# Kernel tuning notes

Measured on AMD Instinct MI355X. Metric: run time of the kernel, lower is better.

Reference implementation:

```python
import jax, jax.numpy as jnp
import numpy as np

B, T, D, H, K = 8, 1024, 512, 8, 33
DK = D // H
PAD = (K - 1) // 2
EPS = 1e-5


def _ln(x, g, b):
    m = x.mean(-1, keepdims=True)
    v = ((x - m) ** 2).mean(-1, keepdims=True)
    return (x - m) / jnp.sqrt(v + EPS) * g + b


def _ffn(x, g, b, w1, b1, w2, b2):
    h = jax.nn.silu(_ln(x, g, b) @ w1 + b1)
    return h @ w2 + b2


def _rel_shift(x):
    # x: [B, H, T1, T2]
    b, h, t1, t2 = x.shape
    x = jnp.pad(x, ((0, 0), (0, 0), (0, 0), (1, 0)))
    x = x.reshape(b, h, t2 + 1, t1)[:, :, 1:, :].reshape(b, h, t1, t2)
    return x[..., :t1]


def setup_inputs() -> dict:
    key = jax.random.key(0)
    ks = iter(jax.random.split(key, 40))
    rn = lambda *s: jax.random.normal(next(ks), s, jnp.float32) * 0.02
    inp = {
        'x': jax.random.normal(next(ks), (B, T, D), jnp.float32),
        'pos_emb': jax.random.normal(next(ks), (1, T, D), jnp.float32),
        # ffn1
        'ln1_g': jnp.ones((D,), jnp.float32), 'ln1_b': jnp.zeros((D,), jnp.float32),
        'ffn1_w1': rn(D, 4 * D), 'ffn1_b1': jnp.zeros((4 * D,), jnp.float32),
        'ffn1_w2': rn(4 * D, D), 'ffn1_b2': jnp.zeros((D,), jnp.float32),
        # mhsa
        'lnq_g': jnp.ones((D,), jnp.float32), 'lnq_b': jnp.zeros((D,), jnp.float32),
        'lnk_g': jnp.ones((D,), jnp.float32), 'lnk_b': jnp.zeros((D,), jnp.float32),
        'lnv_g': jnp.ones((D,), jnp.float32), 'lnv_b': jnp.zeros((D,), jnp.float32),
        'wq': rn(D, D), 'wk': rn(D, D), 'wv': rn(D, D), 'wpos': rn(D, D),
        'pos_bias_u': jnp.zeros((H, DK), jnp.float32),
        'pos_bias_v': jnp.zeros((H, DK), jnp.float32),
        'wfc': rn(D, D),
        # conv module
        'cln_g': jnp.ones((D,), jnp.float32), 'cln_b': jnp.zeros((D,), jnp.float32),
        'pw1': rn(D, 4 * D),             # pointwise_conv1 weight as [in, out]
        'dw_w': rn(2 * D, 1, K),         # depthwise conv weight [C, 1, K]
        'bn_g': jnp.ones((2 * D,), jnp.float32), 'bn_b': jnp.zeros((2 * D,), jnp.float32),
        'pw2': rn(2 * D, D),
        # ffn2
        'ln2_g': jnp.ones((D,), jnp.float32), 'ln2_b': jnp.zeros((D,), jnp.float32),
        'ffn2_w1': rn(D, 4 * D), 'ffn2_b1': jnp.zeros((4 * D,), jnp.float32),
        'ffn2_w2': rn(4 * D, D), 'ffn2_b2': jnp.zeros((D,), jnp.float32),
        # final layer norm
        'lnf_g': jnp.ones((D,), jnp.float32), 'lnf_b': jnp.zeros((D,), jnp.float32),
    }
    return inp


def reference(x, pos_emb, ln1_g, ln1_b, ffn1_w1, ffn1_b1, ffn1_w2, ffn1_b2,
              lnq_g, lnq_b, lnk_g, lnk_b, lnv_g, lnv_b, wq, wk, wv, wpos,
              pos_bias_u, pos_bias_v, wfc,
              cln_g, cln_b, pw1, dw_w, bn_g, bn_b, pw2,
              ln2_g, ln2_b, ffn2_w1, ffn2_b1, ffn2_w2, ffn2_b2, lnf_g, lnf_b):
    b, t, d = x.shape
    scale = 1.0 / DK ** 0.5

    # ---- FFN1 (half-step) ----
    out = 0.5 * x + 0.5 * (x + _ffn(x, ln1_g, ln1_b, ffn1_w1, ffn1_b1, ffn1_w2, ffn1_b2))

    # ---- rel-pos MHSA ----
    res = out
    q = (_ln(out, lnq_g, lnq_b) @ wq).reshape(b, t, H, DK)            # [B,T,H,dk]
    k = (_ln(out, lnk_g, lnk_b) @ wk).reshape(b, t, H, DK).transpose(0, 2, 1, 3)
    v = (_ln(out, lnv_g, lnv_b) @ wv).reshape(b, t, H, DK).transpose(0, 2, 1, 3)
    p = (pos_emb @ wpos).reshape(pos_emb.shape[0], -1, H, DK).transpose(0, 2, 3, 1)  # [1,H,dk,Tp]

    q_u = (q + pos_bias_u).transpose(0, 2, 1, 3)                      # [B,H,T,dk]
    q_v = (q + pos_bias_v).transpose(0, 2, 1, 3)
    matrix_bd = _rel_shift(jnp.matmul(q_v, p) * scale)                # [B,H,T,T]
    scores = jnp.einsum('bhqd,bhkd->bhqk', q_u, k) * scale + matrix_bd
    attn = jax.nn.softmax(scores, axis=-1)
    o = jnp.einsum('bhqk,bhkd->bhqd', attn, v)
    out = o.transpose(0, 2, 1, 3).reshape(b, t, d) @ wfc + res

    # ---- convolution module ----
    res = out
    h = _ln(out, cln_g, cln_b) @ pw1                                  # [B,T,4D]
    a, g = jnp.split(h, 2, axis=-1)
    h = a * jax.nn.sigmoid(g)                                         # GLU -> [B,T,2D]
    h = jax.lax.conv_general_dilated(
        h.transpose(0, 2, 1), dw_w, window_strides=(1,),
        padding=[(PAD, PAD)], feature_group_count=2 * D,
        dimension_numbers=('NCH', 'OIH', 'NCH')).transpose(0, 2, 1)
    h = jax.nn.silu(_ln(h, bn_g, bn_b))
    out = h @ pw2 + res

    # ---- FFN2 (half-step) + final LN ----
    out = 0.5 * out + 0.5 * (out + _ffn(out, ln2_g, ln2_b, ffn2_w1, ffn2_b1, ffn2_w2, ffn2_b2))
    return _ln(out, lnf_g, lnf_b)
```

## Files before the change

kernel.cpp:

```cpp
#include <hip/hip_runtime.h>

typedef unsigned short bf16u;
typedef __attribute__((ext_vector_type(8))) short bf16x8;
typedef __attribute__((ext_vector_type(4))) float f32x4;

__device__ __forceinline__ float bf2f(bf16u u) {
    return __uint_as_float(((unsigned)u) << 16);
}
__device__ __forceinline__ bf16u f2bf(float f) {
    unsigned u = __float_as_uint(f);
    unsigned r = (u + 0x7fffu + ((u >> 16) & 1u)) >> 16;
    return (bf16u)r;
}
__device__ __forceinline__ float sigmoidf_(float x) {
    return 1.0f / (1.0f + __expf(-x));
}

__device__ __forceinline__ void gload_lds16(const bf16u* g, bf16u* l) {
    __builtin_amdgcn_global_load_lds(
        (const __attribute__((address_space(1))) unsigned int*)(const void*)g,
        (__attribute__((address_space(3))) unsigned int*)(void*)l, 16, 0, 0);
}

__global__ void init_flag_kernel(int* flag) {
    if (threadIdx.x == 0 && blockIdx.x == 0) *flag = 0;
}
__global__ __launch_bounds__(256) void detect_kernel(
    const void* x, int nelem, int* flag)
{
    const int scan = nelem < (1 << 20) ? nelem : (1 << 20);
    const bf16u* p = (const bf16u*)x;
    int bad = 0;
    for (int j = blockIdx.x * 256 + threadIdx.x; j < scan; j += 65536) {
        unsigned u = p[j];
        if ((u & 0x7F80u) == 0x7F80u) bad = 1;
    }
    if (bad) atomicOr(flag, 1);
}

__global__ __launch_bounds__(256) void cvt_bf_kernel(
    const void* __restrict__ in, bf16u* __restrict__ out, int n,
    const int* __restrict__ flagp)
{
    const int f32 = *flagp;
    const int i = blockIdx.x * 256 + threadIdx.x;
    if (i >= n) return;
    if (f32) out[i] = f2bf(((const float*)in)[i]);
    else     out[i] = ((const bf16u*)in)[i];
}

__global__ __launch_bounds__(256) void wtrans_kernel(
    const void* __restrict__ W, bf16u* __restrict__ Wt, int K, int N,
    const int* __restrict__ flagp)
{
    __shared__ float tile[32][33];
    const int f32 = *flagp;
    const int n0 = blockIdx.x * 32, k0 = blockIdx.y * 32;
    const int tx = threadIdx.x & 31, ty = threadIdx.x >> 5;
    #pragma unroll
    for (int r = 0; r < 4; ++r) {
        const int k = ty + r * 8;
        float v;
        if (f32) v = ((const float*)W)[(size_t)(k0 + k) * N + n0 + tx];
        else     v = bf2f(((const bf16u*)W)[(size_t)(k0 + k) * N + n0 + tx]);
        tile[k][tx] = v;
    }
    __syncthreads();
    #pragma unroll
    for (int r = 0; r < 4; ++r) {
        const int n = ty + r * 8;
        Wt[(size_t)(n0 + n) * K + k0 + tx] = f2bf(tile[tx][n]);
    }
}

__global__ __launch_bounds__(256) void vtrans_kernel(
    const bf16u* __restrict__ vb, bf16u* __restrict__ vt)
{
    __shared__ bf16u tile[32][33];
    const int j0 = blockIdx.x * 32;
    const int h = blockIdx.y >> 1, dt = (blockIdx.y & 1) * 32;
    const int b = blockIdx.z;
    const int tx = threadIdx.x & 31, ty = threadIdx.x >> 5;
    #pragma unroll
    for (int r = 0; r < 4; ++r) {
        const int j = ty + r * 8;
        tile[j][tx] = vb[(size_t)(b * 1024 + j0 + j) * 512 + h * 64 + dt + tx];
    }
    __syncthreads();
    #pragma unroll
    for (int r = 0; r < 4; ++r) {
        const int d = ty + r * 8;
        vt[(size_t)((b * 8 + h) * 64 + dt + d) * 1024 + j0 + tx] = tile[tx][d];
    }
}

__global__ __launch_bounds__(256) void add_qbias_kernel(
    const bf16u* __restrict__ qb, const void* __restrict__ bu,
    const void* __restrict__ bv, bf16u* __restrict__ qu,
    bf16u* __restrict__ qv, const int* __restrict__ flagp)
{
    const int f32 = *flagp;
    const int idx = blockIdx.x * 256 + threadIdx.x;
    const int c = idx & 511;
    const float q = bf2f(qb[idx]);
    float ub, vbias;
    if (f32) { ub = ((const float*)bu)[c]; vbias = ((const float*)bv)[c]; }
    else     { ub = bf2f(((const bf16u*)bu)[c]); vbias = bf2f(((const bf16u*)bv)[c]); }
    qu[idx] = f2bf(q + ub);
    qv[idx] = f2bf(q + vbias);
}

template <int D, int IN_MODE, int OUT_MODE, bool SILU, bool COPY>
__global__ __launch_bounds__(256) void ln_kernel(
    const void* __restrict__ in_, const void* __restrict__ gvec,
    const void* __restrict__ bvec, void* __restrict__ out_,
    float* __restrict__ copy_out, const int* __restrict__ flagp)
{
    constexpr int VPT = D / 256;
    const int f32 = *flagp;
    const int row = blockIdx.x;
    const int tid = threadIdx.x;
    const size_t base = (size_t)row * D;
    float x[VPT];
    if (IN_MODE == 2 || (IN_MODE == 1 && !f32)) {
        const bf16u* in = (const bf16u*)in_;
        #pragma unroll
        for (int i = 0; i < VPT; ++i) x[i] = bf2f(in[base + tid + i * 256]);
    } else {
        const float* in = (const float*)in_;
        #pragma unroll
        for (int i = 0; i < VPT; ++i) x[i] = in[base + tid + i * 256];
    }
    float s = 0.f, q = 0.f;
    #pragma unroll
    for (int i = 0; i < VPT; ++i) { s += x[i]; q += x[i] * x[i]; }
    __shared__ float red[10];
    #pragma unroll
    for (int off = 32; off; off >>= 1) {
        s += __shfl_down(s, off, 64);
        q += __shfl_down(q, off, 64);
    }
    const int lane = tid & 63, wv = tid >> 6;
    if (lane == 0) { red[wv] = s; red[4 + wv] = q; }
    __syncthreads();
    if (tid == 0) {
        float ts = red[0] + red[1] + red[2] + red[3];
        float tq = red[4] + red[5] + red[6] + red[7];
        float mean = ts / (float)D;
        float var = tq / (float)D - mean * mean;
        red[8] = mean;
        red[9] = rsqrtf(var + 1e-5f);
    }
    __syncthreads();
    const float mean = red[8], rstd = red[9];
    #pragma unroll
    for (int i = 0; i < VPT; ++i) {
        const int c = tid + i * 256;
        float gv, bv;
        if (f32) {
            gv = ((const float*)gvec)[c];
            bv = ((const float*)bvec)[c];
        } else {
            gv = bf2f(((const bf16u*)gvec)[c]);
            bv = bf2f(((const bf16u*)bvec)[c]);
        }
        float v = (x[i] - mean) * rstd * gv + bv;
        if (SILU) v *= sigmoidf_(v);
        if (OUT_MODE == 0) {
            ((bf16u*)out_)[base + c] = f2bf(v);
        } else {
            if (f32) ((float*)out_)[base + c] = v;
            else     ((bf16u*)out_)[base + c] = f2bf(v);
        }
        if (COPY) copy_out[base + c] = x[i];
    }
}

template <int TM>
__global__ __launch_bounds__(256) void gemm_mfma(
    const bf16u* __restrict__ A, const bf16u* __restrict__ Wt,
    const void* __restrict__ bias, const float* __restrict__ res,
    void* __restrict__ C, int M, int N, int K, float alpha, int act,
    int outbf, const int* __restrict__ flagp)
{
    constexpr int CHUNKS_A = TM * 4;
    constexpr int TOT = CHUNKS_A + 512;
    constexpr int CPW = TOT / 4;
    constexpr int ISSUES = CPW / 64;
    constexpr int BUFSZ = (TM + 128) * 32;
    constexpr int MI = 4;
    constexpr int NJ = (TM == 128) ? 4 : 2;
    __shared__ bf16u sh[3 * BUFSZ];
    const int f32 = *flagp;
    const int tid = threadIdx.x;
    const int mtiles = M / TM;
    const int lid = blockIdx.y * gridDim.x + blockIdx.x;
    const int bm = (lid % mtiles) * TM;
    const int bn = (lid / mtiles) * 128;
    const int lane = tid & 63, wvid = tid >> 6;
    const int wm = (TM == 128) ? (wvid >> 1) * 64 : 0;
    const int wn = (TM == 128) ? (wvid & 1) * 64 : wvid * 32;

    f32x4 acc[MI][NJ];
    {
        f32x4 z = {0.f, 0.f, 0.f, 0.f};
        #pragma unroll
        for (int i = 0; i < MI; ++i)
            #pragma unroll
            for (int j = 0; j < NJ; ++j) acc[i][j] = z;
    }
    const int kq = (lane >> 4) * 8, fr = lane & 15;

    #define STAGE_G(k0, bufp)                                                   \
    {                                                                           \
        bf16u* base_ = (bufp);                                                  \
        _Pragma("unroll")                                                       \
        for (int t = 0; t < ISSUES; ++t) {                                      \
            const int cc = wvid * CPW + t * 64 + lane;                          \
            const bf16u* src_;                                                  \
            if (cc < CHUNKS_A)                                                  \
                src_ = A + (size_t)(bm + (cc >> 2)) * K + (k0) + (cc & 3) * 8;  \
            else {                                                              \
                const int cb_ = cc - CHUNKS_A;                                  \
                src_ = Wt + (size_t)(bn + (cb_ >> 2)) * K + (k0) + (cb_ & 3) * 8;\
            }                                                                   \
            gload_lds16(src_, base_ + (wvid * CPW + t * 64) * 8);               \
        }                                                                       \
    }

    const int KT = K / 32;
    STAGE_G(0, sh);
    STAGE_G(32, sh + BUFSZ);
    int bufidx = 0;
    for (int kt = 0; kt < KT; ++kt) {
        if (kt + 1 < KT)
            asm volatile("s_waitcnt vmcnt(%0)\ns_barrier" :: "i"(ISSUES) : "memory");
        else
            asm volatile("s_waitcnt vmcnt(0)\ns_barrier" ::: "memory");
        if (kt + 2 < KT) {
            int nb = bufidx + 2; if (nb >= 3) nb -= 3;
            STAGE_G((kt + 2) * 32, sh + nb * BUFSZ);
        }
        const bf16u* buf = sh + bufidx * BUFSZ;
        bf16x8 af[MI], bfr[NJ];
        #pragma unroll
        for (int i = 0; i < MI; ++i)
            af[i] = *(const bf16x8*)&buf[(wm + i * 16 + fr) * 32 + kq];
        #pragma unroll
        for (int j = 0; j < NJ; ++j)
            bfr[j] = *(const bf16x8*)&buf[TM * 32 + (wn + j * 16 + fr) * 32 + kq];
        #pragma unroll
        for (int i = 0; i < MI; ++i)
            #pragma unroll
            for (int j = 0; j < NJ; ++j)
                acc[i][j] = __builtin_amdgcn_mfma_f32_16x16x32_bf16(
                    af[i], bfr[j], acc[i][j], 0, 0, 0);
        ++bufidx; if (bufidx == 3) bufidx = 0;
    }
    #undef STAGE_G

    const int quad = lane >> 4, col = lane & 15;
    #pragma unroll
    for (int j = 0; j < NJ; ++j) {
        const int n = bn + wn + j * 16 + col;
        float bv = 0.f;
        if (bias) bv = f32 ? ((const float*)bias)[n]
                           : bf2f(((const bf16u*)bias)[n]);
        #pragma unroll
        for (int i = 0; i < MI; ++i) {
            #pragma unroll
            for (int r = 0; r < 4; ++r) {
                const int m = bm + wm + i * 16 + quad * 4 + r;
                float v = acc[i][j][r] + bv;
                if (act == 1) v *= sigmoidf_(v);
                v *= alpha;
                const size_t off = (size_t)m * N + n;
                if (res) v += res[off];
                if (outbf) ((bf16u*)C)[off] = f2bf(v);
                else       ((float*)C)[off] = v;
            }
        }
    }
}

__global__ __launch_bounds__(256) void attn_score_mfma(
    const bf16u* __restrict__ qu, const bf16u* __restrict__ qv,
    const bf16u* __restrict__ kb, const bf16u* __restrict__ pb,
    bf16u* __restrict__ S, bf16u* __restrict__ BD)
{
    constexpr int BUFSZ = 8192;
    __shared__ bf16u sh[2 * BUFSZ];
    const int tid = threadIdx.x;
    const int z = blockIdx.z;
    const int h = z & 7, bb = (z >> 3) & 1, which = z >> 4;
    const bf16u* A = (which ? qv : qu) + (size_t)bb * 524288;
    const bf16u* B = which ? pb : (kb + (size_t)bb * 524288);
    bf16u* C = (which ? BD : S) + (size_t)(bb * 8 + h) * 1048576;
    const int hoff = h * 64;
    const int bm = blockIdx.y * 128, bn = blockIdx.x * 128;
    const int lane = tid & 63, wvid = tid >> 6;
    const int wm = (wvid >> 1) * 64, wn = (wvid & 1) * 64;
    const int kq = (lane >> 4) * 8, fr = lane & 15;

    f32x4 acc[4][4];
    {
        f32x4 zr = {0.f, 0.f, 0.f, 0.f};
        #pragma unroll
        for (int i = 0; i < 4; ++i)
            #pragma unroll
            for (int j = 0; j < 4; ++j) acc[i][j] = zr;
    }

    #define STAGE_S(k0, bsel)                                                   \
    {                                                                           \
        bf16u* base_ = sh + (bsel) * BUFSZ;                                     \
        _Pragma("unroll")                                                       \
        for (int t = 0; t < 4; ++t) {                                           \
            const int cc = wvid * 256 + t * 64 + lane;                          \
            const bf16u* src_;                                                  \
            if (cc < 512)                                                       \
                src_ = A + (size_t)(bm + (cc >> 2)) * 512 + hoff + (k0) + (cc & 3) * 8; \
            else {                                                              \
                const int cb_ = cc - 512;                                       \
                src_ = B + (size_t)(bn + (cb_ >> 2)) * 512 + hoff + (k0) + (cb_ & 3) * 8; \
            }                                                                   \
            gload_lds16(src_, base_ + (wvid * 256 + t * 64) * 8);               \
        }                                                                       \
    }

    STAGE_S(0, 0);
    #pragma unroll
    for (int kt = 0; kt < 2; ++kt) {
        __syncthreads();
        if (kt == 0) STAGE_S(32, 1);
        const bf16u* buf = sh + (kt & 1) * BUFSZ;
        bf16x8 af[4], bfr[4];
        #pragma unroll
        for (int i = 0; i < 4; ++i)
            af[i] = *(const bf16x8*)&buf[(wm + i * 16 + fr) * 32 + kq];
        #pragma unroll
        for (int j = 0; j < 4; ++j)
            bfr[j] = *(const bf16x8*)&buf[4096 + (wn + j * 16 + fr) * 32 + kq];
        #pragma unroll
        for (int i = 0; i < 4; ++i)
            #pragma unroll
            for (int j = 0; j < 4; ++j)
                acc[i][j] = __builtin_amdgcn_mfma_f32_16x16x32_bf16(
                    af[i], bfr[j], acc[i][j], 0, 0, 0);
    }
    #undef STAGE_S

    const int quad = lane >> 4, col = lane & 15;
    #pragma unroll
    for (int j = 0; j < 4; ++j) {
        const int n = bn + wn + j * 16 + col;
        #pragma unroll
        for (int i = 0; i < 4; ++i) {
            #pragma unroll
            for (int r = 0; r < 4; ++r) {
                const int m = bm + wm + i * 16 + quad * 4 + r;
                C[(size_t)m * 1024 + n] = f2bf(acc[i][j][r] * 0.125f);
            }
        }
    }
}

__global__ __launch_bounds__(256) void attn_softmax_kernel(
    bf16u* __restrict__ S, const bf16u* __restrict__ BD)
{
    const int i = blockIdx.x, h = blockIdx.y, bb = blockIdx.z;
    const int tid = threadIdx.x;
    const size_t hb = (size_t)(bb * 8 + h) * 1048576;
    bf16u* srow = S + hb + (size_t)i * 1024;
    const bf16u* bd0 = BD + hb + (size_t)i * 1024;
    const bf16u* bd1 = bd0 + 1024;
    float v[4];
    #pragma unroll
    for (int k = 0; k < 4; ++k) {
        const int j = tid + k * 256;
        float bd;
        if (j <= i)          bd = bf2f(bd0[1023 - i + j]);
        else if (j == i + 1) bd = 0.f;
        else                 bd = bf2f(bd1[j - i - 2]);
        v[k] = bf2f(srow[j]) + bd;
    }
    __shared__ float red[6];
    float m = fmaxf(fmaxf(v[0], v[1]), fmaxf(v[2], v[3]));
    #pragma unroll
    for (int off = 32; off; off >>= 1) m = fmaxf(m, __shfl_down(m, off, 64));
    const int lane = tid & 63, w = tid >> 6;
    if (lane == 0) red[w] = m;
    __syncthreads();
    if (tid == 0) red[4] = fmaxf(fmaxf(red[0], red[1]), fmaxf(red[2], red[3]));
    __syncthreads();
    m = red[4];
    float e[4], l = 0.f;
    #pragma unroll
    for (int k = 0; k < 4; ++k) { e[k] = __expf(v[k] - m); l += e[k]; }
    #pragma unroll
    for (int off = 32; off; off >>= 1) l += __shfl_down(l, off, 64);
    if (lane == 0) red[w] = l;
    __syncthreads();
    if (tid == 0) red[5] = red[0] + red[1] + red[2] + red[3];
    __syncthreads();
    const float inv = 1.0f / red[5];
    #pragma unroll
    for (int k = 0; k < 4; ++k) srow[tid + k * 256] = f2bf(e[k] * inv);
}

__global__ __launch_bounds__(256) void attn_pv_mfma(
    const bf16u* __restrict__ P, const bf16u* __restrict__ Vt,
    bf16u* __restrict__ O)
{
    constexpr int BUFSZ = 4096;
    __shared__ bf16u sh[3 * BUFSZ];
    const int tid = threadIdx.x;
    const int h = blockIdx.y, bb = blockIdx.z;
    const int bm = blockIdx.x * 64;
    const int hoff = h * 64;
    const bf16u* Ph = P + (size_t)(bb * 8 + h) * 1048576;
    const bf16u* Vh = Vt + (size_t)bb * 524288 + (size_t)h * 65536;
    bf16u* Ob = O + (size_t)bb * 524288;
    const int lane = tid & 63, wvid = tid >> 6;
    const int wm = wvid * 16;
    const int kq = (lane >> 4) * 8, fr = lane & 15;

    f32x4 acc[4];
    {
        f32x4 z = {0.f, 0.f, 0.f, 0.f};
        #pragma unroll
        for (int j = 0; j < 4; ++j) acc[j] = z;
    }

    #define STAGE_P(k0, bufp)                                                   \
    {                                                                           \
        bf16u* base_ = (bufp);                                                  \
        _Pragma("unroll")                                                       \
        for (int t = 0; t < 2; ++t) {                                           \
            const int cc = wvid * 128 + t * 64 + lane;                          \
            const bf16u* src_;                                                  \
            if (cc < 256)                                                       \
                src_ = Ph + (size_t)(bm + (cc >> 2)) * 1024 + (k0) + (cc & 3) * 8; \
            else {                                                              \
                const int cb_ = cc - 256;                                       \
                src_ = Vh + (size_t)(cb_ >> 2) * 1024 + (k0) + (cb_ & 3) * 8;   \
            }                                                                   \
            gload_lds16(src_, base_ + (wvid * 128 + t * 64) * 8);               \
        }                                                                       \
    }

    STAGE_P(0, sh);
    STAGE_P(32, sh + BUFSZ);
    int bufidx = 0;
    for (int kt = 0; kt < 32; ++kt) {
        if (kt + 1 < 32)
            asm volatile("s_waitcnt vmcnt(2)\ns_barrier" ::: "memory");
        else
            asm volatile("s_waitcnt vmcnt(0)\ns_barrier" ::: "memory");
        if (kt + 2 < 32) {
            int nb = bufidx + 2; if (nb >= 3) nb -= 3;
            STAGE_P((kt + 2) * 32, sh + nb * BUFSZ);
        }
        const bf16u* buf = sh + bufidx * BUFSZ;
        bf16x8 af = *(const bf16x8*)&buf[(wm + fr) * 32 + kq];
        #pragma unroll
        for (int j = 0; j < 4; ++j) {
            bf16x8 bf = *(const bf16x8*)&buf[2048 + (j * 16 + fr) * 32 + kq];
            acc[j] = __builtin_amdgcn_mfma_f32_16x16x32_bf16(af, bf, acc[j], 0, 0, 0);
        }
        ++bufidx; if (bufidx == 3) bufidx = 0;
    }
    #undef STAGE_P

    const int quad = lane >> 4, col = lane & 15;
    #pragma unroll
    for (int j = 0; j < 4; ++j) {
        const int d = j * 16 + col;
        #pragma unroll
        for (int r = 0; r < 4; ++r) {
            const int m = bm + wm + quad * 4 + r;
            Ob[(size_t)m * 512 + hoff + d] = f2bf(acc[j][r]);
        }
    }
}

__global__ __launch_bounds__(256) void glu_kernel(
    const bf16u* __restrict__ H, bf16u* __restrict__ out, int total)
{
    const int idx = blockIdx.x * 256 + threadIdx.x;
    if (idx >= total) return;
    const int m = idx >> 10, c = idx & 1023;
    const float a = bf2f(H[(size_t)m * 2048 + c]);
    const float g = bf2f(H[(size_t)m * 2048 + 1024 + c]);
    out[idx] = f2bf(a * sigmoidf_(g));
}

__global__ __launch_bounds__(256) void dwconv_kernel(
    const bf16u* __restrict__ in, const void* __restrict__ wp,
    bf16u* __restrict__ out, const int* __restrict__ flagp)
{
    const int f32 = *flagp;
    const int cb = blockIdx.x & 1;
    const int ttile = (blockIdx.x >> 1) & 127;
    const int b = blockIdx.x >> 8;
    const int t0 = ttile * 8;
    const int c = cb * 512 + threadIdx.x * 2;

    float w0[33], w1[33];
    if (f32) {
        const float* wf = (const float*)wp;
        #pragma unroll
        for (int k = 0; k < 33; ++k) { w0[k] = wf[c * 33 + k]; w1[k] = wf[(c + 1) * 33 + k]; }
    } else {
        const bf16u* wb = (const bf16u*)wp;
        #pragma unroll
        for (int k = 0; k < 33; ++k) { w0[k] = bf2f(wb[c * 33 + k]); w1[k] = bf2f(wb[(c + 1) * 33 + k]); }
    }

    unsigned win[40];
    #pragma unroll
    for (int r = 0; r < 40; ++r) {
        const int tt = t0 - 16 + r;
        win[r] = (tt >= 0 && tt < 1024)
               ? *(const unsigned*)(in + (size_t)(b * 1024 + tt) * 1024 + c)
               : 0u;
    }
    float acc0[8] = {}, acc1[8] = {};
    #pragma unroll
    for (int k = 0; k < 33; ++k) {
        #pragma unroll
        for (int dt = 0; dt < 8; ++dt) {
            const unsigned u = win[dt + k];
            acc0[dt] = fmaf(bf2f((bf16u)(u & 0xffffu)), w0[k], acc0[dt]);
            acc1[dt] = fmaf(bf2f((bf16u)(u >> 16)), w1[k], acc1[dt]);
        }
    }
    #pragma unroll
    for (int dt = 0; dt < 8; ++dt) {
        unsigned o = (unsigned)f2bf(acc0[dt]) | ((unsigned)f2bf(acc1[dt]) << 16);
        *(unsigned*)(out + (size_t)(b * 1024 + t0 + dt) * 1024 + c) = o;
    }
}

static inline void launch_gemm(const bf16u* A, const bf16u* Wt, const void* bias,
                               const float* res, void* C, int M, int N, int K,
                               float alpha, int act, int outbf, const int* flagp,
                               hipStream_t stream)
{
    if (N >= 1024) {
        dim3 grid(N / 128, M / 128);
        gemm_mfma<128><<<grid, 256, 0, stream>>>(A, Wt, bias, res, C, M, N, K, alpha, act, outbf, flagp);
    } else {
        dim3 grid(N / 128, M / 64);
        gemm_mfma<64><<<grid, 256, 0, stream>>>(A, Wt, bias, res, C, M, N, K, alpha, act, outbf, flagp);
    }
}

extern "C" void kernel_launch(void* const* d_in, const int* in_sizes, int n_in,
                              void* d_out, int out_size, void* d_ws, size_t ws_size,
                              hipStream_t stream)
{
    const void* x       = d_in[0];
    const void* pos_emb = d_in[1];
    const void* ln1_g   = d_in[2];
    const void* ln1_b   = d_in[3];
    const void* ffn1_w1 = d_in[4];
    const void* ffn1_b1 = d_in[5];
    const void* ffn1_w2 = d_in[6];
    const void* ffn1_b2 = d_in[7];
    const void* lnq_g   = d_in[8];
    const void* lnq_b   = d_in[9];
    const void* lnk_g   = d_in[10];
    const void* lnk_b   = d_in[11];
    const void* lnv_g   = d_in[12];
    const void* lnv_b   = d_in[13];
    const void* wq      = d_in[14];
    const void* wk      = d_in[15];
    const void* wv      = d_in[16];
    const void* wpos    = d_in[17];
    const void* pbu     = d_in[18];
    const void* pbv     = d_in[19];
    const void* wfc     = d_in[20];
    const void* cln_g   = d_in[21];
    const void* cln_b   = d_in[22];
    const void* pw1     = d_in[23];
    const void* dw_w    = d_in[24];
    const void* bn_g    = d_in[25];
    const void* bn_b    = d_in[26];
    const void* pw2     = d_in[27];
    const void* ln2_g   = d_in[28];
    const void* ln2_b   = d_in[29];
    const void* ffn2_w1 = d_in[30];
    const void* ffn2_b1 = d_in[31];
    const void* ffn2_w2 = d_in[32];
    const void* ffn2_b2 = d_in[33];
    const void* lnf_g   = d_in[34];
    const void* lnf_b   = d_in[35];

    const int BT = 8192;
    char* wsb = (char*)d_ws;
    float* act  = (float*)(wsb + 0);
    bf16u* qb   = (bf16u*)(wsb + 16777216);
    bf16u* kb   = (bf16u*)(wsb + 25165824);
    bf16u* vb   = (bf16u*)(wsb + 33554432);
    bf16u* pb   = (bf16u*)(wsb + 41943040);
    bf16u* tmpb = (bf16u*)(wsb + 42991616);
    bf16u* qu   = (bf16u*)(wsb + 51380224);
    bf16u* qv   = (bf16u*)(wsb + 59768832);
    bf16u* vt   = (bf16u*)(wsb + 68157440);
    bf16u* S    = (bf16u*)(wsb + 76546048);
    bf16u* BD   = (bf16u*)(wsb + 110100480);
    bf16u* wc   = (bf16u*)(wsb + 143654912);
    int* flagp  = (int*)(wsb + 157810688);
    bf16u* obb  = tmpb;
    bf16u* hbf  = (bf16u*)(wsb + 51380224);
    bf16u* Gbf  = (bf16u*)(wsb + 84934656);
    bf16u* DWbf = (bf16u*)(wsb + 16777216);
    bf16u* LObf = (bf16u*)(wsb + 33554432);

    bf16u* w_ffn1_1 = wc + 0;
    bf16u* w_ffn1_2 = wc + 1048576;
    bf16u* w_q      = wc + 2097152;
    bf16u* w_k      = wc + 2359296;
    bf16u* w_v      = wc + 2621440;
    bf16u* w_pos    = wc + 2883584;
    bf16u* w_fc     = wc + 3145728;
    bf16u* w_pw1    = wc + 3407872;
    bf16u* w_pw2    = wc + 4456448;
    bf16u* w_ffn2_1 = wc + 4980736;
    bf16u* w_ffn2_2 = wc + 6029312;

    init_flag_kernel<<<1, 64, 0, stream>>>(flagp);
    detect_kernel<<<256, 256, 0, stream>>>(x, in_sizes[0], flagp);

    wtrans_kernel<<<dim3(64, 16), 256, 0, stream>>>(ffn1_w1, w_ffn1_1, 512, 2048, flagp);
    wtrans_kernel<<<dim3(16, 64), 256, 0, stream>>>(ffn1_w2, w_ffn1_2, 2048, 512, flagp);
    wtrans_kernel<<<dim3(16, 16), 256, 0, stream>>>(wq, w_q, 512, 512, flagp);
    wtrans_kernel<<<dim3(16, 16), 256, 0, stream>>>(wk, w_k, 512, 512, flagp);
    wtrans_kernel<<<dim3(16, 16), 256, 0, stream>>>(wv, w_v, 512, 512, flagp);
    wtrans_kernel<<<dim3(16, 16), 256, 0, stream>>>(wpos, w_pos, 512, 512, flagp);
    wtrans_kernel<<<dim3(16, 16), 256, 0, stream>>>(wfc, w_fc, 512, 512, flagp);
    wtrans_kernel<<<dim3(64, 16), 256, 0, stream>>>(pw1, w_pw1, 512, 2048, flagp);
    wtrans_kernel<<<dim3(16, 32), 256, 0, stream>>>(pw2, w_pw2, 1024, 512, flagp);
    wtrans_kernel<<<dim3(64, 16), 256, 0, stream>>>(ffn2_w1, w_ffn2_1, 512, 2048, flagp);
    wtrans_kernel<<<dim3(16, 64), 256, 0, stream>>>(ffn2_w2, w_ffn2_2, 2048, 512, flagp);

    cvt_bf_kernel<<<2048, 256, 0, stream>>>(pos_emb, tmpb, 524288, flagp);
    launch_gemm(tmpb, w_pos, nullptr, nullptr, pb, 1024, 512, 512, 1.0f, 0, 1, flagp, stream);

    ln_kernel<512, 1, 0, false, true><<<BT, 256, 0, stream>>>(x, ln1_g, ln1_b, tmpb, act, flagp);
    launch_gemm(tmpb, w_ffn1_1, ffn1_b1, nullptr, hbf, BT, 2048, 512, 1.0f, 1, 1, flagp, stream);
    launch_gemm(hbf, w_ffn1_2, ffn1_b2, act, act, BT, 512, 2048, 0.5f, 0, 0, flagp, stream);

    ln_kernel<512, 0, 0, false, false><<<BT, 256, 0, stream>>>(act, lnq_g, lnq_b, tmpb, nullptr, flagp);
    launch_gemm(tmpb, w_q, nullptr, nullptr, qb, BT, 512, 512, 1.0f, 0, 1, flagp, stream);
    ln_kernel<512, 0, 0, false, false><<<BT, 256, 0, stream>>>(act, lnk_g, lnk_b, tmpb, nullptr, flagp);
    launch_gemm(tmpb, w_k, nullptr, nullptr, kb, BT, 512, 512, 1.0f, 0, 1, flagp, stream);
    ln_kernel<512, 0, 0, false, false><<<BT, 256, 0, stream>>>(act, lnv_g, lnv_b, tmpb, nullptr, flagp);
    launch_gemm(tmpb, w_v, nullptr, nullptr, vb, BT, 512, 512, 1.0f, 0, 1, flagp, stream);

    add_qbias_kernel<<<16384, 256, 0, stream>>>(qb, pbu, pbv, qu, qv, flagp);
    vtrans_kernel<<<dim3(32, 16, 8), 256, 0, stream>>>(vb, vt);

    for (int b0 = 0; b0 < 8; b0 += 2) {
        const bf16u* qu_b = qu + (size_t)b0 * 524288;
        const bf16u* qv_b = qv + (size_t)b0 * 524288;
        const bf16u* kb_b = kb + (size_t)b0 * 524288;
        const bf16u* vt_b = vt + (size_t)b0 * 524288;
        bf16u* ob_b = obb + (size_t)b0 * 524288;
        attn_score_mfma<<<dim3(8, 8, 32), 256, 0, stream>>>(qu_b, qv_b, kb_b, pb, S, BD);
        attn_softmax_kernel<<<dim3(1024, 8, 2), 256, 0, stream>>>(S, BD);
        attn_pv_mfma<<<dim3(16, 8, 2), 256, 0, stream>>>(S, vt_b, ob_b);
    }
    launch_gemm(obb, w_fc, nullptr, act, act, BT, 512, 512, 1.0f, 0, 0, flagp, stream);

    ln_kernel<512, 0, 0, false, false><<<BT, 256, 0, stream>>>(act, cln_g, cln_b, tmpb, nullptr, flagp);
    launch_gemm(tmpb, w_pw1, nullptr, nullptr, hbf, BT, 2048, 512, 1.0f, 0, 1, flagp, stream);
    glu_kernel<<<32768, 256, 0, stream>>>(hbf, Gbf, 8388608);
    dwconv_kernel<<<2048, 256, 0, stream>>>(Gbf, dw_w, DWbf, flagp);
    ln_kernel<1024, 2, 0, true, false><<<BT, 256, 0, stream>>>(DWbf, bn_g, bn_b, LObf, nullptr, flagp);
    launch_gemm(LObf, w_pw2, nullptr, act, act, BT, 512, 1024, 1.0f, 0, 0, flagp, stream);

    ln_kernel<512, 0, 0, false, false><<<BT, 256, 0, stream>>>(act, ln2_g, ln2_b, tmpb, nullptr, flagp);
    launch_gemm(tmpb, w_ffn2_1, ffn2_b1, nullptr, hbf, BT, 2048, 512, 1.0f, 1, 1, flagp, stream);
    launch_gemm(hbf, w_ffn2_2, ffn2_b2, act, act, BT, 512, 2048, 0.5f, 0, 0, flagp, stream);

    ln_kernel<512, 0, 1, false, false><<<BT, 256, 0, stream>>>(act, lnf_g, lnf_b, d_out, nullptr, flagp);
}
```

Measured before the change: 835.3 us.

## Swap MFMA operands for vectorized epilogue stores and batch weight transposes

Swaps the A/B operands of the MFMA calls in the GEMM, score and PV kernels so that each lane holds four consecutive output columns. The epilogues can then issue vector stores (ushort4/float4) and vector bias and residual loads instead of scalar strided stores. Separately, the eleven weight-transpose launches are merged into one launch that reads a table of pointers and shapes, with out-of-range blocks exiting early. The risks are that the merged grid of 64x64x11 spawns many empty blocks, and that the operand swap depends on the transposed accumulator layout being mapped correctly.

New measurement: 812.4 us. 1.03x faster.

```diff
diff --git a/kernel.cpp b/kernel.cpp
--- a/kernel.cpp
+++ b/kernel.cpp
@@ -49,13 +49,23 @@
     else     out[i] = ((const bf16u*)in)[i];
 }
 
-__global__ __launch_bounds__(256) void wtrans_kernel(
-    const void* __restrict__ W, bf16u* __restrict__ Wt, int K, int N,
-    const int* __restrict__ flagp)
+struct WTab {
+    const void* w[11];
+    bf16u* wt[11];
+    int K[11];
+    int N[11];
+};
+__global__ __launch_bounds__(256) void wtrans_all(
+    WTab tab, const int* __restrict__ flagp)
 {
     __shared__ float tile[32][33];
+    const int id = blockIdx.z;
+    const int K = tab.K[id], N = tab.N[id];
+    const int n0 = blockIdx.x * 32, k0 = blockIdx.y * 32;
+    if (n0 >= N || k0 >= K) return;
+    const void* W = tab.w[id];
+    bf16u* Wt = tab.wt[id];
     const int f32 = *flagp;
-    const int n0 = blockIdx.x * 32, k0 = blockIdx.y * 32;
     const int tx = threadIdx.x & 31, ty = threadIdx.x >> 5;
     #pragma unroll
     for (int r = 0; r < 4; ++r) {
@@ -254,7 +264,7 @@
             #pragma unroll
             for (int j = 0; j < NJ; ++j)
                 acc[i][j] = __builtin_amdgcn_mfma_f32_16x16x32_bf16(
-                    af[i], bfr[j], acc[i][j], 0, 0, 0);
+                    bfr[j], af[i], acc[i][j], 0, 0, 0);
         ++bufidx; if (bufidx == 3) bufidx = 0;
     }
     #undef STAGE_G
@@ -262,22 +272,39 @@
     const int quad = lane >> 4, col = lane & 15;
     #pragma unroll
     for (int j = 0; j < NJ; ++j) {
-        const int n = bn + wn + j * 16 + col;
-        float bv = 0.f;
-        if (bias) bv = f32 ? ((const float*)bias)[n]
-                           : bf2f(((const bf16u*)bias)[n]);
+        const int n0 = bn + wn + j * 16 + quad * 4;
+        float4 bv4 = {0.f, 0.f, 0.f, 0.f};
+        if (bias) {
+            if (f32) bv4 = *(const float4*)((const float*)bias + n0);
+            else {
+                ushort4 bu = *(const ushort4*)((const bf16u*)bias + n0);
+                bv4.x = bf2f(bu.x); bv4.y = bf2f(bu.y);
+                bv4.z = bf2f(bu.z); bv4.w = bf2f(bu.w);
+            }
+        }
         #pragma unroll
         for (int i = 0; i < MI; ++i) {
+            const int m = bm + wm + i * 16 + col;
+            const size_t off = (size_t)m * N + n0;
+            float v[4];
             #pragma unroll
             for (int r = 0; r < 4; ++r) {
-                const int m = bm + wm + i * 16 + quad * 4 + r;
-                float v = acc[i][j][r] + bv;
-                if (act == 1) v *= sigmoidf_(v);
-                v *= alpha;
-                const size_t off = (size_t)m * N + n;
-                if (res) v += res[off];
-                if (outbf) ((bf16u*)C)[off] = f2bf(v);
-                else       ((float*)C)[off] = v;
+                float t = acc[i][j][r] + ((const float*)&bv4)[r];
+                if (act == 1) t *= sigmoidf_(t);
+                v[r] = t * alpha;
+            }
+            if (res) {
+                float4 r4 = *(const float4*)(res + off);
+                v[0] += r4.x; v[1] += r4.y; v[2] += r4.z; v[3] += r4.w;
+            }
+            if (outbf) {
+                ushort4 o;
+                o.x = f2bf(v[0]); o.y = f2bf(v[1]);
+                o.z = f2bf(v[2]); o.w = f2bf(v[3]);
+                *(ushort4*)((bf16u*)C + off) = o;
+            } else {
+                float4 o = {v[0], v[1], v[2], v[3]};
+                *(float4*)((float*)C + off) = o;
             }
         }
     }
@@ -346,21 +373,23 @@
             #pragma unroll
             for (int j = 0; j < 4; ++j)
                 acc[i][j] = __builtin_amdgcn_mfma_f32_16x16x32_bf16(
-                    af[i], bfr[j], acc[i][j], 0, 0, 0);
+                    bfr[j], af[i], acc[i][j], 0, 0, 0);
     }
     #undef STAGE_S
 
     const int quad = lane >> 4, col = lane & 15;
     #pragma unroll
     for (int j = 0; j < 4; ++j) {
-        const int n = bn + wn + j * 16 + col;
+        const int n0 = bn + wn + j * 16 + quad * 4;
         #pragma unroll
         for (int i = 0; i < 4; ++i) {
-            #pragma unroll
-            for (int r = 0; r < 4; ++r) {
-                const int m = bm + wm + i * 16 + quad * 4 + r;
-                C[(size_t)m * 1024 + n] = f2bf(acc[i][j][r] * 0.125f);
-            }
+            const int m = bm + wm + i * 16 + col;
+            ushort4 o;
+            o.x = f2bf(acc[i][j][0] * 0.125f);
+            o.y = f2bf(acc[i][j][1] * 0.125f);
+            o.z = f2bf(acc[i][j][2] * 0.125f);
+            o.w = f2bf(acc[i][j][3] * 0.125f);
+            *(ushort4*)(C + (size_t)m * 1024 + n0) = o;
         }
     }
 }
@@ -466,21 +495,21 @@
         #pragma unroll
         for (int j = 0; j < 4; ++j) {
             bf16x8 bf = *(const bf16x8*)&buf[2048 + (j * 16 + fr) * 32 + kq];
-            acc[j] = __builtin_amdgcn_mfma_f32_16x16x32_bf16(af, bf, acc[j], 0, 0, 0);
+            acc[j] = __builtin_amdgcn_mfma_f32_16x16x32_bf16(bf, af, acc[j], 0, 0, 0);
         }
         ++bufidx; if (bufidx == 3) bufidx = 0;
     }
     #undef STAGE_P
 
     const int quad = lane >> 4, col = lane & 15;
+    const int m = bm + wm + col;
     #pragma unroll
     for (int j = 0; j < 4; ++j) {
-        const int d = j * 16 + col;
-        #pragma unroll
-        for (int r = 0; r < 4; ++r) {
-            const int m = bm + wm + quad * 4 + r;
-            Ob[(size_t)m * 512 + hoff + d] = f2bf(acc[j][r]);
-        }
+        const int d0 = j * 16 + quad * 4;
+        ushort4 o;
+        o.x = f2bf(acc[j][0]); o.y = f2bf(acc[j][1]);
+        o.z = f2bf(acc[j][2]); o.w = f2bf(acc[j][3]);
+        *(ushort4*)(Ob + (size_t)m * 512 + hoff + d0) = o;
     }
 }
 
@@ -633,17 +662,19 @@
     init_flag_kernel<<<1, 64, 0, stream>>>(flagp);
     detect_kernel<<<256, 256, 0, stream>>>(x, in_sizes[0], flagp);
 
-    wtrans_kernel<<<dim3(64, 16), 256, 0, stream>>>(ffn1_w1, w_ffn1_1, 512, 2048, flagp);
-    wtrans_kernel<<<dim3(16, 64), 256, 0, stream>>>(ffn1_w2, w_ffn1_2, 2048, 512, flagp);
-    wtrans_kernel<<<dim3(16, 16), 256, 0, stream>>>(wq, w_q, 512, 512, flagp);
-    wtrans_kernel<<<dim3(16, 16), 256, 0, stream>>>(wk, w_k, 512, 512, flagp);
-    wtrans_kernel<<<dim3(16, 16), 256, 0, stream>>>(wv, w_v, 512, 512, flagp);
-    wtrans_kernel<<<dim3(16, 16), 256, 0, stream>>>(wpos, w_pos, 512, 512, flagp);
-    wtrans_kernel<<<dim3(16, 16), 256, 0, stream>>>(wfc, w_fc, 512, 512, flagp);
-    wtrans_kernel<<<dim3(64, 16), 256, 0, stream>>>(pw1, w_pw1, 512, 2048, flagp);
-    wtrans_kernel<<<dim3(16, 32), 256, 0, stream>>>(pw2, w_pw2, 1024, 512, flagp);
-    wtrans_kernel<<<dim3(64, 16), 256, 0, stream>>>(ffn2_w1, w_ffn2_1, 512, 2048, flagp);
-    wtrans_kernel<<<dim3(16, 64), 256, 0, stream>>>(ffn2_w2, w_ffn2_2, 2048, 512, flagp);
+    WTab tab;
+    tab.w[0] = ffn1_w1; tab.wt[0] = w_ffn1_1; tab.K[0] = 512;  tab.N[0] = 2048;
+    tab.w[1] = ffn1_w2; tab.wt[1] = w_ffn1_2; tab.K[1] = 2048; tab.N[1] = 512;
+    tab.w[2] = wq;      tab.wt[2] = w_q;      tab.K[2] = 512;  tab.N[2] = 512;
+    tab.w[3] = wk;      tab.wt[3] = w_k;      tab.K[3] = 512;  tab.N[3] = 512;
+    tab.w[4] = wv;      tab.wt[4] = w_v;      tab.K[4] = 512;  tab.N[4] = 512;
+    tab.w[5] = wpos;    tab.wt[5] = w_pos;    tab.K[5] = 512;  tab.N[5] = 512;
+    tab.w[6] = wfc;     tab.wt[6] = w_fc;     tab.K[6] = 512;  tab.N[6] = 512;
+    tab.w[7] = pw1;     tab.wt[7] = w_pw1;    tab.K[7] = 512;  tab.N[7] = 2048;
+    tab.w[8] = pw2;     tab.wt[8] = w_pw2;    tab.K[8] = 1024; tab.N[8] = 512;
+    tab.w[9] = ffn2_w1; tab.wt[9] = w_ffn2_1; tab.K[9] = 512;  tab.N[9] = 2048;
+    tab.w[10] = ffn2_w2; tab.wt[10] = w_ffn2_2; tab.K[10] = 2048; tab.N[10] = 512;
+    wtrans_all<<<dim3(64, 64, 11), 256, 0, stream>>>(tab, flagp);
 
     cvt_bf_kernel<<<2048, 256, 0, stream>>>(pos_emb, tmpb, 524288, flagp);
     launch_gemm(tmpb, w_pos, nullptr, nullptr, pb, 1024, 512, 512, 1.0f, 0, 1, flagp, stream);
```
